# Kernel optimization log

Measured on AMD Instinct MI355X. Metric: run time of the kernel, lower is better.

## Reference

```python
import jax, jax.numpy as jnp
import numpy as np


def conv2d(x, w, b, pad):
    # x: NCHW, w: OIHW, stride 1, symmetric padding
    y = jax.lax.conv_general_dilated(
        x, w, window_strides=(1, 1), padding=[(pad, pad), (pad, pad)],
        dimension_numbers=('NCHW', 'OIHW', 'NCHW'))
    return y + b[None, :, None, None]


def setup_inputs() -> dict:
    key = jax.random.key(0)
    ks = jax.random.split(key, 10)
    N, Cin, H, W = 8, 256, 64, 64
    Cr = 64
    wscale = 0.02  # keep softmax logits moderate
    return {
        'feature_maps': jax.random.normal(ks[0], (N, Cin, H, W), jnp.float32),
        'global_channel_output': jax.random.normal(ks[1], (N, Cin, H, W), jnp.float32),
        'wq': jax.random.normal(ks[2], (Cr, Cin, 3, 3), jnp.float32) * wscale,
        'bq': jnp.zeros((Cr,), jnp.float32),
        'wk': jax.random.normal(ks[3], (Cr, Cin, 5, 5), jnp.float32) * wscale,
        'bk': jnp.zeros((Cr,), jnp.float32),
        'wv': jax.random.normal(ks[4], (Cr, Cin, 7, 7), jnp.float32) * wscale,
        'bv': jnp.zeros((Cr,), jnp.float32),
        'watt': jax.random.normal(ks[5], (Cin, Cr, 1, 1), jnp.float32) * wscale,
        'batt': jnp.zeros((Cin,), jnp.float32),
    }


def reference(feature_maps, global_channel_output, wq, bq, wk, bk, wv, bv, watt, batt):
    N, Cin, H, W = feature_maps.shape
    HW = H * W
    q = conv2d(feature_maps, wq, bq, 1).reshape(N, -1, HW)  # (N, Cr, HW)
    k = conv2d(feature_maps, wk, bk, 2).reshape(N, -1, HW)
    v = conv2d(feature_maps, wv, bv, 3).reshape(N, -1, HW)
    # key^T @ query: (N, HW, HW)
    qk = jnp.einsum('nci,ncj->nij', k, q)
    # GLOBAL softmax over the whole flattened HW*HW matrix per sample
    qk = jax.nn.softmax(qk.reshape(N, -1), axis=-1).reshape(N, HW, HW)
    att = jnp.einsum('nci,nij->ncj', v, qk).reshape(N, -1, H, W)  # (N, Cr, H, W)
    att = conv2d(att, watt, batt, 0)  # (N, Cin, H, W)
    return global_channel_output * att + global_channel_output
```

## Files before the change

### kernel.cpp

```cpp
#include <hip/hip_runtime.h>
#include <math.h>

#define NB 8
#define CIN 256
#define CR 64
#define H 64
#define W 64
#define HW 4096

typedef _Float16 f16;
typedef _Float16 f16x8 __attribute__((ext_vector_type(8)));
typedef _Float16 f16x4 __attribute__((ext_vector_type(4)));
typedef float f32x4 __attribute__((ext_vector_type(4)));

static const size_t QKV = (size_t)NB * CR * HW;

static __device__ __forceinline__ float ex2(float x) {
    return __builtin_amdgcn_exp2f(x);
}

__global__ __launch_bounds__(256) void prep_all(
    const float* __restrict__ wq, const float* __restrict__ wk,
    const float* __restrict__ wv,
    f16* __restrict__ dq, f16* __restrict__ dk, f16* __restrict__ dv)
{
    int b = blockIdx.x;
    const float* src; f16* dst; int KK;
    if (b < 576)       { src = wq; dst = dq; KK = 9; }
    else if (b < 2176) { src = wk; dst = dk; KK = 25; b -= 576; }
    else               { src = wv; dst = dv; KK = 49; b -= 2176; }
    int idx = b * 256 + threadIdx.x;
    int ci = idx & 255;
    int co = (idx >> 8) & 63;
    int off = idx >> 14;
    dst[((size_t)(off * 64 + co)) * 256 + ci] = (f16)src[((size_t)(co * 256 + ci)) * KK + off];
}

__global__ __launch_bounds__(256) void transpose_fm(
    const float* __restrict__ fm, f16* __restrict__ fmT)
{
    const int y = blockIdx.x & 63;
    const int n = blockIdx.x >> 6;
    const int tid = threadIdx.x;
    __shared__ f16x4 tile[64 * 64];
    const int xw = tid & 63;
    const int wv = tid >> 6;
    const float* s0 = fm + ((size_t)n * CIN) * HW + y * W + xw;
#pragma unroll
    for (int cc = 0; cc < 16; ++cc) {
        const int slot = wv * 16 + cc;
        const float* s = s0 + (size_t)(slot * 4) * HW;
        f16x4 pk;
#pragma unroll
        for (int e = 0; e < 4; ++e) pk[e] = (f16)s[(size_t)e * HW];
        tile[xw * 64 + (slot ^ xw)] = pk;
    }
    __syncthreads();
    f16x4* dst = (f16x4*)fmT + ((size_t)n * HW + y * W) * 64;
#pragma unroll
    for (int it = 0; it < 16; ++it) {
        const int idx = tid + it * 256;
        const int x = idx >> 6;
        const int slot = idx & 63;
        dst[x * 64 + slot] = tile[x * 64 + (slot ^ x)];
    }
}

template<int K, int LAYOUT>
static __device__ __forceinline__ void conv_body(
    const f16* __restrict__ fmT, const f16* __restrict__ wT,
    const float* __restrict__ bias, f16* __restrict__ dst, float oscale,
    unsigned char* smem, int bid0)
{
    constexpr int P = K / 2;
    constexpr int XBYTES = 2 * 72 * 128;
    unsigned char* Xl = smem;
    unsigned char* Wl = smem + XBYTES;

    const int bid = (bid0 & 7) * 32 + (bid0 >> 3);
    const int n  = bid >> 5;
    const int y0 = (bid & 31) * 2;
    const int tid = threadIdx.x;
    const int w = tid >> 6;
    const int lane = tid & 63;
    const int r  = w >> 2;
    const int h  = (w >> 1) & 1;
    const int sw = w & 1;
    const int lm = lane & 15;
    const int g  = lane >> 4;

    if (tid < 128) {
        const int sl = tid >> 6;
        const int cidx = (tid >> 3) & 7;
        const int chunk = tid & 7;
        const int col = (cidx < P) ? cidx : (64 + cidx);
        *(uint4*)(Xl + (size_t)(sl * 72 + col) * 128 + chunk * 16) = uint4{0, 0, 0, 0};
    }

    f32x4 acc[2][4];
#pragma unroll
    for (int i = 0; i < 2; ++i)
#pragma unroll
        for (int jx = 0; jx < 4; ++jx) acc[i][jx] = f32x4{0.f, 0.f, 0.f, 0.f};

    for (int dy = 0; dy < K; ++dy) {
        for (int ch = 0; ch < 4; ++ch) {
            __syncthreads();
#pragma unroll
            for (int p = 0; p < 2; ++p) {
                const int idx = tid + p * 512;
                const int sl = idx >> 9;
                const int x = (idx >> 3) & 63;
                const int chunk = idx & 7;
                const int iy = y0 + sl + dy - P;
                uint4 val = uint4{0, 0, 0, 0};
                if (iy >= 0 && iy < H)
                    val = *(const uint4*)(fmT + ((size_t)n * HW + iy * 64 + x) * 256 +
                                          ch * 64 + chunk * 8);
                *(uint4*)(Xl + (size_t)(sl * 72 + x + P) * 128 +
                          ((chunk * 16) ^ (((x + P) & 7) << 4))) = val;
            }
#pragma unroll
            for (int p = 0; p < K; ++p) {
                const int idx = tid + p * 512;
                const int cig = idx & 7;
                const int co  = (idx >> 3) & 63;
                const int dx  = idx >> 9;
                const f16* s = wT + ((size_t)((dy * K + dx) * 64 + co)) * 256 + ch * 64 + cig * 8;
                *(uint4*)(Wl + (size_t)(dx * 64 + co) * 128 +
                          ((cig * 16) ^ ((co & 7) << 4))) = *(const uint4*)s;
            }
            __syncthreads();
#pragma unroll
            for (int dx = 0; dx < K; ++dx) {
                f16x8 a[2], b[4];
#pragma unroll
                for (int cf = 0; cf < 2; ++cf) {
                    const int co = h * 32 + cf * 16 + lm;
                    a[cf] = *(const f16x8*)(Wl + (size_t)(dx * 64 + co) * 128 +
                                            ((sw * 64 + g * 16) ^ ((co & 7) << 4)));
                }
#pragma unroll
                for (int xf = 0; xf < 4; ++xf) {
                    const int col = xf * 16 + lm + dx;
                    b[xf] = *(const f16x8*)(Xl + (size_t)(r * 72 + col) * 128 +
                                            ((sw * 64 + g * 16) ^ ((col & 7) << 4)));
                }
#pragma unroll
                for (int cf = 0; cf < 2; ++cf)
#pragma unroll
                    for (int xf = 0; xf < 4; ++xf)
                        acc[cf][xf] = __builtin_amdgcn_mfma_f32_16x16x32_f16(
                            a[cf], b[xf], acc[cf][xf], 0, 0, 0);
            }
        }
    }

    __syncthreads();
    {
        const int mslot = r * 2 + h;
        if (sw == 1) {
#pragma unroll
            for (int cf = 0; cf < 2; ++cf)
#pragma unroll
                for (int xf = 0; xf < 4; ++xf)
                    *(f32x4*)(smem + (size_t)(mslot * 64 + lane) * 128 +
                              (((cf * 4 + xf) * 16) ^ ((lane & 7) << 4))) = acc[cf][xf];
        }
        __syncthreads();
        if (sw == 0) {
#pragma unroll
            for (int cf = 0; cf < 2; ++cf)
#pragma unroll
                for (int xf = 0; xf < 4; ++xf)
                    acc[cf][xf] += *(const f32x4*)(smem + (size_t)(mslot * 64 + lane) * 128 +
                                                   (((cf * 4 + xf) * 16) ^ ((lane & 7) << 4)));
        }
    }

    if (sw == 0) {
        const int y = y0 + r;
#pragma unroll
        for (int cf = 0; cf < 2; ++cf) {
            const float4 bv = *(const float4*)(bias + h * 32 + cf * 16 + g * 4);
            if (LAYOUT == 0) {
#pragma unroll
                for (int xf = 0; xf < 4; ++xf) {
                    f16x4 pk;
#pragma unroll
                    for (int e = 0; e < 4; ++e)
                        pk[e] = (f16)((acc[cf][xf][e] + ((const float*)&bv)[e]) * oscale);
                    *(f16x4*)(dst + ((size_t)n * HW + y * W + xf * 16 + lm) * 64 +
                              h * 32 + cf * 16 + g * 4) = pk;
                }
            } else {
#pragma unroll
                for (int e = 0; e < 4; ++e) {
                    const int co = h * 32 + cf * 16 + g * 4 + e;
#pragma unroll
                    for (int xf = 0; xf < 4; ++xf)
                        dst[((size_t)(n * CR + co)) * HW + y * W + xf * 16 + lm] =
                            (f16)((acc[cf][xf][e] + ((const float*)&bv)[e]) * oscale);
                }
            }
        }
    }
}

__global__ __launch_bounds__(512) void conv_all(
    const f16* __restrict__ fmT,
    const f16* __restrict__ wTq, const f16* __restrict__ wTk, const f16* __restrict__ wTv,
    const float* __restrict__ bq, const float* __restrict__ bk, const float* __restrict__ bv,
    f16* __restrict__ qT, f16* __restrict__ kT, f16* __restrict__ vvb, float log2e)
{
    __shared__ __align__(16) unsigned char smem[2 * 72 * 128 + 7 * 64 * 128];
    const int b = blockIdx.x;
    if (b < 256)      conv_body<3, 0>(fmT, wTq, bq, qT, log2e, smem, b);
    else if (b < 512) conv_body<5, 0>(fmT, wTk, bk, kT, 1.0f, smem, b - 256);
    else              conv_body<7, 1>(fmT, wTv, bv, vvb, 1.0f, smem, b - 512);
}

__global__ __launch_bounds__(256, 2) void attn_mfma(
    const f16* __restrict__ qT, const f16* __restrict__ kT, const f16* __restrict__ vv,
    f16* __restrict__ attu, float* __restrict__ Mcol, float* __restrict__ Zcol)
{
    const int bid0 = blockIdx.x;
    const int bid = (bid0 & 7) * 64 + (bid0 >> 3);
    const int jt = bid & 63;
    const int n  = bid >> 6;
    const int j0 = jt * 64;
    const int tid = threadIdx.x;
    const int wv = tid >> 6;
    const int lane = tid & 63;
    const int lm = lane & 15;
    const int g  = lane >> 4;
    const int key = (lm & 7) << 4;

    __shared__ __align__(16) f16 Qt[64 * 64];
    __shared__ __align__(16) f16 Kt[64 * 64];
    __shared__ __align__(16) f16 Vt[64 * 64];

    {
        const int r = tid >> 2;
        const f16* src = qT + ((size_t)n * HW + j0 + r) * 64;
#pragma unroll
        for (int h = 0; h < 2; ++h) {
            const int ch = (tid & 3) * 2 + h;
            *(uint4*)((char*)Qt + r * 128 + ((ch * 16) ^ ((r & 7) << 4))) =
                *(const uint4*)(src + ch * 8);
        }
    }

    float m = -1e30f, z = 0.f;
    f32x4 accp[4];
#pragma unroll
    for (int c = 0; c < 4; ++c) accp[c] = f32x4{0.f, 0.f, 0.f, 0.f};

    for (int it = 0; it < 64; ++it) {
        const int i0 = it * 64;
        __syncthreads();
        {
            const int r = tid >> 2;
            const f16* ks = kT + ((size_t)n * HW + i0 + r) * 64;
            const f16* vs = vv + ((size_t)n * CR + r) * HW + i0;
#pragma unroll
            for (int h = 0; h < 2; ++h) {
                const int ch = (tid & 3) * 2 + h;
                *(uint4*)((char*)Kt + r * 128 + ((ch * 16) ^ ((r & 7) << 4))) =
                    *(const uint4*)(ks + ch * 8);
                *(uint4*)((char*)Vt + r * 128 + ((ch * 16) ^ ((r & 7) << 4))) =
                    *(const uint4*)(vs + ch * 8);
            }
        }
        __syncthreads();

        f32x4 sacc[4];
#pragma unroll
        for (int f = 0; f < 4; ++f) sacc[f] = f32x4{0.f, 0.f, 0.f, 0.f};
#pragma unroll
        for (int ks2 = 0; ks2 < 2; ++ks2) {
            const int off = (ks2 * 64 + g * 16);
            const f16x8 B = *(const f16x8*)((char*)Qt + (wv * 16 + lm) * 128 + (off ^ key));
#pragma unroll
            for (int f = 0; f < 4; ++f) {
                const f16x8 A = *(const f16x8*)((char*)Kt + (f * 16 + lm) * 128 + (off ^ key));
                sacc[f] = __builtin_amdgcn_mfma_f32_16x16x32_f16(A, B, sacc[f], 0, 0, 0);
            }
        }

        const float mA = fmaxf(fmaxf(sacc[0][0], sacc[0][1]), fmaxf(sacc[0][2], sacc[0][3]));
        const float mB = fmaxf(fmaxf(sacc[1][0], sacc[1][1]), fmaxf(sacc[1][2], sacc[1][3]));
        const float mC = fmaxf(fmaxf(sacc[2][0], sacc[2][1]), fmaxf(sacc[2][2], sacc[2][3]));
        const float mD = fmaxf(fmaxf(sacc[3][0], sacc[3][1]), fmaxf(sacc[3][2], sacc[3][3]));
        float mt = fmaxf(fmaxf(mA, mB), fmaxf(mC, mD));
        mt = fmaxf(mt, __shfl_xor(mt, 16));
        mt = fmaxf(mt, __shfl_xor(mt, 32));
        if (__ballot(mt > m)) {
            const float mnew = fmaxf(m, mt);
            const float rsc = ex2(m - mnew);
            z *= rsc;
#pragma unroll
            for (int cf = 0; cf < 4; ++cf) {
                accp[cf][0] *= rsc; accp[cf][1] *= rsc;
                accp[cf][2] *= rsc; accp[cf][3] *= rsc;
            }
            m = mnew;
        }
        f16x4 p16[4];
        float zp[4];
#pragma unroll
        for (int f = 0; f < 4; ++f) {
            const float e0 = ex2(sacc[f][0] - m), e1 = ex2(sacc[f][1] - m);
            const float e2 = ex2(sacc[f][2] - m), e3 = ex2(sacc[f][3] - m);
            zp[f] = (e0 + e1) + (e2 + e3);
            p16[f][0] = (f16)e0; p16[f][1] = (f16)e1;
            p16[f][2] = (f16)e2; p16[f][3] = (f16)e3;
        }
        float zt = (zp[0] + zp[1]) + (zp[2] + zp[3]);
        zt += __shfl_xor(zt, 16);
        zt += __shfl_xor(zt, 32);
        z += zt;

#pragma unroll
        for (int cf = 0; cf < 4; ++cf) {
#pragma unroll
            for (int f = 0; f < 4; ++f) {
                const f16x4 A = *(const f16x4*)((char*)Vt + (cf * 16 + lm) * 128 +
                                                ((f * 32 + g * 8) ^ key));
                accp[cf] = __builtin_amdgcn_mfma_f32_16x16x16f16(A, p16[f], accp[cf], 0, 0, 0);
            }
        }
    }

    const int j = j0 + wv * 16 + lm;
    const size_t jbase = ((size_t)n * HW + j) * 64;
#pragma unroll
    for (int cf = 0; cf < 4; ++cf) {
        f16x4 pk;
#pragma unroll
        for (int e = 0; e < 4; ++e) pk[e] = (f16)accp[cf][e];
        *(f16x4*)(attu + jbase + cf * 16 + g * 4) = pk;
    }
    if (g == 0) {
        Mcol[(size_t)n * HW + j] = m;
        Zcol[(size_t)n * HW + j] = z;
    }
}

__global__ __launch_bounds__(256) void reduce_kernel(
    const float* __restrict__ Mcol, const float* __restrict__ Zcol,
    float* __restrict__ Mn, float* __restrict__ Zn)
{
    const int n = blockIdx.x;
    const int tid = threadIdx.x;
    __shared__ float red[256];

    float lm = -1e30f;
    for (int j = tid; j < HW; j += 256) lm = fmaxf(lm, Mcol[(size_t)n * HW + j]);
    red[tid] = lm; __syncthreads();
    for (int s = 128; s > 0; s >>= 1) {
        if (tid < s) red[tid] = fmaxf(red[tid], red[tid + s]);
        __syncthreads();
    }
    const float M = red[0];
    __syncthreads();

    float ls = 0.f;
    for (int j = tid; j < HW; j += 256)
        ls += Zcol[(size_t)n * HW + j] * ex2(Mcol[(size_t)n * HW + j] - M);
    red[tid] = ls; __syncthreads();
    for (int s = 128; s > 0; s >>= 1) {
        if (tid < s) red[tid] += red[tid + s];
        __syncthreads();
    }
    if (tid == 0) { Mn[n] = M; Zn[n] = red[0]; }
}

__global__ __launch_bounds__(512) void final_mfma(
    const f16* __restrict__ attu, const float* __restrict__ Mcol,
    const float* __restrict__ Mn, const float* __restrict__ Zn,
    const float* __restrict__ watt, const float* __restrict__ batt,
    const float* __restrict__ gco, float* __restrict__ out)
{
    __shared__ __align__(16) f16 Wl[256 * 64];
    __shared__ __align__(16) f16 Al[128 * 64];

    const int bid0 = blockIdx.x;
    const int bid = (bid0 & 7) * 32 + (bid0 >> 3);
    const int n  = bid >> 5;
    const int p0 = (bid & 31) * 128;
    const int tid = threadIdx.x;
    const int wv = tid >> 6;
    const int lane = tid & 63;
    const int lm = lane & 15;
    const int g  = lane >> 4;

#pragma unroll
    for (int t = 0; t < 8; ++t) {
        const int idx = tid + t * 512;
        const int co = idx >> 4;
        const int ch = idx & 15;
        const float4 w4 = *(const float4*)(watt + (size_t)co * 64 + ch * 4);
        f16x4 pk;
        pk[0] = (f16)w4.x; pk[1] = (f16)w4.y; pk[2] = (f16)w4.z; pk[3] = (f16)w4.w;
        *(f16x4*)((char*)Wl + co * 128 + ((ch * 8) ^ ((co & 7) << 4))) = pk;
    }
#pragma unroll
    for (int t = 0; t < 4; ++t) {
        const int idx = tid + t * 512;
        const int pp = idx >> 3;
        const int ch = idx & 7;
        *(uint4*)((char*)Al + pp * 128 + ((ch * 16) ^ ((pp & 7) << 4))) =
            *(const uint4*)(attu + ((size_t)n * HW + p0 + pp) * 64 + ch * 8);
    }
    __syncthreads();

    f32x4 acc[2][8];
#pragma unroll
    for (int cf = 0; cf < 2; ++cf)
#pragma unroll
        for (int pf = 0; pf < 8; ++pf) acc[cf][pf] = f32x4{0.f, 0.f, 0.f, 0.f};

#pragma unroll
    for (int ks = 0; ks < 2; ++ks) {
        const int off = ks * 64 + g * 16;
        f16x8 A[2], B[8];
#pragma unroll
        for (int cf = 0; cf < 2; ++cf) {
            const int co = wv * 32 + cf * 16 + lm;
            A[cf] = *(const f16x8*)((char*)Wl + co * 128 + (off ^ ((co & 7) << 4)));
        }
#pragma unroll
        for (int pf = 0; pf < 8; ++pf) {
            const int pp = pf * 16 + lm;
            B[pf] = *(const f16x8*)((char*)Al + pp * 128 + (off ^ ((pp & 7) << 4)));
        }
#pragma unroll
        for (int cf = 0; cf < 2; ++cf)
#pragma unroll
            for (int pf = 0; pf < 8; ++pf)
                acc[cf][pf] = __builtin_amdgcn_mfma_f32_16x16x32_f16(
                    A[cf], B[pf], acc[cf][pf], 0, 0, 0);
    }

    const float M = Mn[n];
    const float Zi = 1.f / Zn[n];
    float ecol[8];
#pragma unroll
    for (int pf = 0; pf < 8; ++pf)
        ecol[pf] = ex2(Mcol[(size_t)n * HW + p0 + pf * 16 + lm] - M) * Zi;

#pragma unroll
    for (int cf = 0; cf < 2; ++cf) {
#pragma unroll
        for (int e = 0; e < 4; ++e) {
            const int co = wv * 32 + cf * 16 + g * 4 + e;
            const float bb = batt[co] + 1.f;
            const float* gsrc = gco + (size_t)(n * CIN + co) * HW + p0 + lm;
            float* dstp = out + (size_t)(n * CIN + co) * HW + p0 + lm;
#pragma unroll
            for (int pf = 0; pf < 8; ++pf) {
                const float gvv = gsrc[pf * 16];
                dstp[pf * 16] = gvv * (acc[cf][pf][e] * ecol[pf] + bb);
            }
        }
    }
}

extern "C" void kernel_launch(void* const* d_in, const int* in_sizes, int n_in,
                              void* d_out, int out_size, void* d_ws, size_t ws_size,
                              hipStream_t stream)
{
    (void)in_sizes; (void)n_in; (void)out_size; (void)ws_size;
    const float* fm   = (const float*)d_in[0];
    const float* gco  = (const float*)d_in[1];
    const float* wq   = (const float*)d_in[2];
    const float* bq   = (const float*)d_in[3];
    const float* wk   = (const float*)d_in[4];
    const float* bk   = (const float*)d_in[5];
    const float* wv   = (const float*)d_in[6];
    const float* bv   = (const float*)d_in[7];
    const float* watt = (const float*)d_in[8];
    const float* batt = (const float*)d_in[9];
    float* out = (float*)d_out;

    f16* qT   = (f16*)out;
    f16* kT   = qT + QKV;
    f16* vvb  = kT + QKV;
    f16* fmT  = vvb + QKV;

    unsigned char* wsb = (unsigned char*)d_ws;
    f16* wTq = (f16*)(wsb);
    f16* wTk = (f16*)(wsb + 294912);
    f16* wTv = (f16*)(wsb + 1114112);
    f16* attu = (f16*)(wsb + 2719744);
    float* Mcol = (float*)(wsb + 6914048);
    float* Zcol = (float*)(wsb + 7045120);
    float* Mn   = (float*)(wsb + 7176192);
    float* Zn   = (float*)(wsb + 7176224);

    const float LOG2E = 1.4426950408889634f;

    prep_all<<<5312, 256, 0, stream>>>(wq, wk, wv, wTq, wTk, wTv);
    transpose_fm<<<NB * 64, 256, 0, stream>>>(fm, fmT);

    conv_all<<<768, 512, 0, stream>>>(fmT, wTq, wTk, wTv, bq, bk, bv,
                                      qT, kT, vvb, LOG2E);

    attn_mfma<<<NB * 64, 256, 0, stream>>>(qT, kT, vvb, attu, Mcol, Zcol);
    reduce_kernel<<<NB, 256, 0, stream>>>(Mcol, Zcol, Mn, Zn);
    final_mfma<<<256, 512, 0, stream>>>(attu, Mcol, Mn, Zn, watt, batt, gco, out);
}
```

Before: 220.9 us.

## Pre-swizzle conv weights into MFMA fragment order and read them directly from global

```diff
diff --git a/kernel.cpp b/kernel.cpp
--- a/kernel.cpp
+++ b/kernel.cpp
@@ -26,14 +26,22 @@
 {
     int b = blockIdx.x;
     const float* src; f16* dst; int KK;
-    if (b < 576)       { src = wq; dst = dq; KK = 9; }
-    else if (b < 2176) { src = wk; dst = dk; KK = 25; b -= 576; }
-    else               { src = wv; dst = dv; KK = 49; b -= 2176; }
-    int idx = b * 256 + threadIdx.x;
-    int ci = idx & 255;
-    int co = (idx >> 8) & 63;
-    int off = idx >> 14;
-    dst[((size_t)(off * 64 + co)) * 256 + ci] = (f16)src[((size_t)(co * 256 + ci)) * KK + off];
+    if (b < 72)       { src = wq; dst = dq; KK = 9; }
+    else if (b < 272) { src = wk; dst = dk; KK = 25; b -= 72; }
+    else              { src = wv; dst = dv; KK = 49; b -= 272; }
+    const int o8 = b * 256 + threadIdx.x;
+    const int lane = o8 & 63;
+    const int hcf2 = (o8 >> 6) & 3;
+    const int sw   = (o8 >> 8) & 1;
+    const int ch   = (o8 >> 9) & 3;
+    const int dxy  = o8 >> 11;
+    const int co  = hcf2 * 16 + (lane & 15);
+    const int ci0 = ch * 64 + sw * 32 + (lane >> 4) * 8;
+    const float* s = src + (size_t)(co * 256 + ci0) * KK + dxy;
+    f16x8 pk;
+#pragma unroll
+    for (int e = 0; e < 8; ++e) pk[e] = (f16)s[(size_t)e * KK];
+    *(f16x8*)(dst + (size_t)o8 * 8) = pk;
 }
 
 __global__ __launch_bounds__(256) void transpose_fm(
@@ -68,14 +76,12 @@
 
 template<int K, int LAYOUT>
 static __device__ __forceinline__ void conv_body(
-    const f16* __restrict__ fmT, const f16* __restrict__ wT,
+    const f16* __restrict__ fmT, const f16* __restrict__ wF,
     const float* __restrict__ bias, f16* __restrict__ dst, float oscale,
     unsigned char* smem, int bid0)
 {
     constexpr int P = K / 2;
-    constexpr int XBYTES = 2 * 72 * 128;
     unsigned char* Xl = smem;
-    unsigned char* Wl = smem + XBYTES;
 
     const int bid = (bid0 & 7) * 32 + (bid0 >> 3);
     const int n  = bid >> 5;
@@ -120,26 +126,15 @@
                 *(uint4*)(Xl + (size_t)(sl * 72 + x + P) * 128 +
                           ((chunk * 16) ^ (((x + P) & 7) << 4))) = val;
             }
-#pragma unroll
-            for (int p = 0; p < K; ++p) {
-                const int idx = tid + p * 512;
-                const int cig = idx & 7;
-                const int co  = (idx >> 3) & 63;
-                const int dx  = idx >> 9;
-                const f16* s = wT + ((size_t)((dy * K + dx) * 64 + co)) * 256 + ch * 64 + cig * 8;
-                *(uint4*)(Wl + (size_t)(dx * 64 + co) * 128 +
-                          ((cig * 16) ^ ((co & 7) << 4))) = *(const uint4*)s;
-            }
             __syncthreads();
 #pragma unroll
             for (int dx = 0; dx < K; ++dx) {
+                const size_t fbase =
+                    ((size_t)(((dy * K + dx) * 4 + ch) * 2 + sw) * 4 + h * 2) * 512;
                 f16x8 a[2], b[4];
 #pragma unroll
-                for (int cf = 0; cf < 2; ++cf) {
-                    const int co = h * 32 + cf * 16 + lm;
-                    a[cf] = *(const f16x8*)(Wl + (size_t)(dx * 64 + co) * 128 +
-                                            ((sw * 64 + g * 16) ^ ((co & 7) << 4)));
-                }
+                for (int cf = 0; cf < 2; ++cf)
+                    a[cf] = *(const f16x8*)(wF + fbase + cf * 512 + lane * 8);
 #pragma unroll
                 for (int xf = 0; xf < 4; ++xf) {
                     const int col = xf * 16 + lm + dx;
@@ -209,15 +204,15 @@
 
 __global__ __launch_bounds__(512) void conv_all(
     const f16* __restrict__ fmT,
-    const f16* __restrict__ wTq, const f16* __restrict__ wTk, const f16* __restrict__ wTv,
+    const f16* __restrict__ wFq, const f16* __restrict__ wFk, const f16* __restrict__ wFv,
     const float* __restrict__ bq, const float* __restrict__ bk, const float* __restrict__ bv,
     f16* __restrict__ qT, f16* __restrict__ kT, f16* __restrict__ vvb, float log2e)
 {
-    __shared__ __align__(16) unsigned char smem[2 * 72 * 128 + 7 * 64 * 128];
+    __shared__ __align__(16) unsigned char smem[32768];
     const int b = blockIdx.x;
-    if (b < 256)      conv_body<3, 0>(fmT, wTq, bq, qT, log2e, smem, b);
-    else if (b < 512) conv_body<5, 0>(fmT, wTk, bk, kT, 1.0f, smem, b - 256);
-    else              conv_body<7, 1>(fmT, wTv, bv, vvb, 1.0f, smem, b - 512);
+    if (b < 256)      conv_body<3, 0>(fmT, wFq, bq, qT, log2e, smem, b);
+    else if (b < 512) conv_body<5, 0>(fmT, wFk, bk, kT, 1.0f, smem, b - 256);
+    else              conv_body<7, 1>(fmT, wFv, bv, vvb, 1.0f, smem, b - 512);
 }
 
 __global__ __launch_bounds__(256, 2) void attn_mfma(
@@ -490,9 +485,9 @@
     f16* fmT  = vvb + QKV;
 
     unsigned char* wsb = (unsigned char*)d_ws;
-    f16* wTq = (f16*)(wsb);
-    f16* wTk = (f16*)(wsb + 294912);
-    f16* wTv = (f16*)(wsb + 1114112);
+    f16* wFq = (f16*)(wsb);
+    f16* wFk = (f16*)(wsb + 294912);
+    f16* wFv = (f16*)(wsb + 1114112);
     f16* attu = (f16*)(wsb + 2719744);
     float* Mcol = (float*)(wsb + 6914048);
     float* Zcol = (float*)(wsb + 7045120);
@@ -501,10 +496,10 @@
 
     const float LOG2E = 1.4426950408889634f;
 
-    prep_all<<<5312, 256, 0, stream>>>(wq, wk, wv, wTq, wTk, wTv);
+    prep_all<<<664, 256, 0, stream>>>(wq, wk, wv, wFq, wFk, wFv);
     transpose_fm<<<NB * 64, 256, 0, stream>>>(fm, fmT);
 
-    conv_all<<<768, 512, 0, stream>>>(fmT, wTq, wTk, wTv, bq, bk, bv,
+    conv_all<<<768, 512, 0, stream>>>(fmT, wFq, wFk, wFv, bq, bk, bv,
                                       qT, kT, vvb, LOG2E);
 
     attn_mfma<<<NB * 64, 256, 0, stream>>>(qT, kT, vvb, attu, Mcol, Zcol);
```

Result: slower. 244.6 us (+10.7%).
